# Optimization experiments

Measured on AMD Instinct MI355X. Metric: run time of the kernel, lower is better.

Reference implementation:

```python
import jax, jax.numpy as jnp
import numpy as np
from jax import lax

T, B, H_IN, H_HID = 2048, 64, 256, 256


def _orth(key, shape):
    a = jax.random.normal(key, shape, jnp.float32)
    if shape[0] >= shape[1]:
        q, _ = jnp.linalg.qr(a)
    else:
        q, _ = jnp.linalg.qr(a.T)
        q = q.T
    return q[: shape[0], : shape[1]].astype(jnp.float32)


def setup_inputs() -> dict:
    key = jax.random.key(0)
    ks = jax.random.split(key, 6)
    x = jax.random.normal(ks[0], (T, B, H_IN), jnp.float32)
    rnn_hxs = jax.random.normal(ks[1], (1, B, H_HID), jnp.float32)
    batch_mask = jax.random.randint(ks[2], (T, B), 0, 2).astype(bool)
    # force column 0 fully valid so pad_packed max length == T (static shape)
    batch_mask = batch_mask.at[:, 0].set(True)
    w_ih = _orth(ks[3], (3 * H_HID, H_IN))   # [3H, H_in] gates r,z,n
    w_hh = _orth(ks[4], (3 * H_HID, H_HID))
    b_ih = jnp.zeros((3 * H_HID,), jnp.float32)  # constant_(0) init
    b_hh = jnp.zeros((3 * H_HID,), jnp.float32)
    return {"x": x, "rnn_hxs": rnn_hxs, "batch_mask": batch_mask,
            "w_ih": w_ih, "w_hh": w_hh, "b_ih": b_ih, "b_hh": b_hh}


def _gru_ragged(x, h0, batch_mask, w_ih, w_hh, b_ih, b_hh):
    Tn, Bn, _ = x.shape
    Hh = h0.shape[-1]
    mask = batch_mask
    lens = mask.sum(0)                      # [B] per-column valid lengths
    # --- gather/pack: move valid steps of each column to the front ---
    rank = jnp.cumsum(mask, axis=0) - mask  # compact position per (t,b)
    rank_m = jnp.where(mask, rank, Tn)      # invalid rows -> dump row Tn
    cols = jnp.broadcast_to(jnp.arange(Bn), (Tn, Bn))
    compact = jnp.zeros((Tn + 1, Bn, x.shape[-1]), x.dtype)
    compact = compact.at[rank_m, cols].set(x)[:Tn]
    # --- GRU over compact sequences; h frozen past each column's length ---
    gi = jnp.einsum('tbi,gi->tbg', compact, w_ih) + b_ih  # [T,B,3H]
    valid = jnp.arange(Tn)[:, None] < lens[None, :]       # [T,B]

    def step(h, inp):
        gi_t, v = inp
        gh = jnp.einsum('bh,gh->bg', h, w_hh) + b_hh
        r = jax.nn.sigmoid(gi_t[:, :Hh] + gh[:, :Hh])
        z = jax.nn.sigmoid(gi_t[:, Hh:2 * Hh] + gh[:, Hh:2 * Hh])
        n = jnp.tanh(gi_t[:, 2 * Hh:] + r * gh[:, 2 * Hh:])
        h_new = (1.0 - z) * n + z * h
        h_out = jnp.where(v[:, None], h_new, h)
        out = jnp.where(v[:, None], h_new, 0.0)  # pad_packed zero padding
        return h_out, out

    hT, scores = lax.scan(step, h0, (gi, valid))  # scores [T,B,Hh]
    # --- masked_scatter: true positions of dest (row-major t,b order)
    # consume consecutive H-rows of the flattened padded scores ---
    mflat = mask.reshape(-1)
    flat_rank = jnp.cumsum(mflat) - mflat            # exclusive cumsum
    src = scores.reshape(Tn * Bn, Hh)
    gathered = src[flat_rank]                        # [T*B, Hh]
    out = jnp.where(mflat[:, None], gathered, 0.0).reshape(Tn, Bn, Hh)
    return out, hT


def reference(x, rnn_hxs, batch_mask, w_ih, w_hh, b_ih, b_hh):
    scores, hT = _gru_ragged(x, rnn_hxs[0], batch_mask, w_ih, w_hh, b_ih, b_hh)
    return scores, hT[None]
```

## Files before the change

### kernel.cpp

```cpp
#include <hip/hip_runtime.h>
#include <cstdint>
#include <cstddef>

#define T_LEN 2048
#define B_N   64
#define H_INP 256
#define H_HID 256
#define G3    768
#define M_ROWS (T_LEN * B_N)
#define SCH   16

typedef _Float16 f16;
typedef _Float16 f16x2 __attribute__((ext_vector_type(2)));
typedef _Float16 f16x8 __attribute__((ext_vector_type(8)));
typedef float    f32x4 __attribute__((ext_vector_type(4)));

static __device__ __forceinline__ float fdot2f(uint32_t a, uint32_t b, float c) {
#if __has_builtin(__builtin_amdgcn_fdot2)
  return __builtin_amdgcn_fdot2(__builtin_bit_cast(f16x2, a),
                                __builtin_bit_cast(f16x2, b), c, false);
#else
  f16x2 av = __builtin_bit_cast(f16x2, a);
  f16x2 bv = __builtin_bit_cast(f16x2, b);
  return c + (float)av.x * (float)bv.x + (float)av.y * (float)bv.y;
#endif
}

__global__ void k_zero(float4* __restrict__ p, int n4) {
  int i = blockIdx.x * blockDim.x + threadIdx.x;
  int stride = gridDim.x * blockDim.x;
  float4 z; z.x = z.y = z.z = z.w = 0.f;
  for (; i < n4; i += stride) p[i] = z;
}

__global__ void k_cvt(const float2* __restrict__ s, f16x2* __restrict__ d, int n2) {
  int i = blockIdx.x * blockDim.x + threadIdx.x;
  int stride = gridDim.x * blockDim.x;
  for (; i < n2; i += stride) {
    float2 v = s[i];
    f16x2 p; p.x = (f16)v.x; p.y = (f16)v.y;
    d[i] = p;
  }
}

__global__ __launch_bounds__(64) void k_prep_col(const int* __restrict__ mask,
                                                 unsigned short* __restrict__ tidx,
                                                 int* __restrict__ lens) {
  const int b = blockIdx.x;
  const int lane = threadIdx.x;
  unsigned short* tp = tidx + b * T_LEN;
  int base = 0;
  for (int c = 0; c < T_LEN / 64; ++c) {
    int t = c * 64 + lane;
    bool m = mask[t * B_N + b] != 0;
    unsigned long long bal = __ballot(m);
    int pc = __popcll(bal & ((1ull << lane) - 1ull));
    if (m) tp[base + pc] = (unsigned short)t;
    base += __popcll(bal);
  }
  if (lane == 0) lens[b] = base;
}

__global__ __launch_bounds__(256) void k_rowcnt(const int* __restrict__ mask,
                                                int* __restrict__ rowcnt) {
  int g = blockIdx.x * 256 + threadIdx.x;
  int t = g >> 6, lane = g & 63;
  bool m = mask[t * B_N + lane] != 0;
  unsigned long long bal = __ballot(m);
  if (lane == 0) rowcnt[t] = __popcll(bal);
}

__global__ __launch_bounds__(512) void k_rowpref(const int* __restrict__ rowcnt,
                                                 int* __restrict__ rowpref,
                                                 int* __restrict__ ntru) {
  const int tid = threadIdx.x;
  const int lane = tid & 63, w = tid >> 6;
  int4 v = ((const int4*)rowcnt)[tid];
  int s = v.x + v.y + v.z + v.w;
  int incl = s;
  for (int d = 1; d < 64; d <<= 1) {
    int t = __shfl_up(incl, d, 64);
    if (lane >= d) incl += t;
  }
  __shared__ int wt[8], wo[8];
  if (lane == 63) wt[w] = incl;
  __syncthreads();
  if (tid == 0) {
    int run = 0;
    for (int i = 0; i < 8; ++i) { wo[i] = run; run += wt[i]; }
    ntru[0] = run;
  }
  __syncthreads();
  int base = wo[w] + incl - s;
  int4 o; o.x = base; o.y = base + v.x; o.z = o.y + v.y; o.w = o.z + v.z;
  ((int4*)rowpref)[tid] = o;
}

__global__ __launch_bounds__(256) void k_inv(const int* __restrict__ mask,
                                             const int* __restrict__ rowpref,
                                             int* __restrict__ inv) {
  int g = blockIdx.x * 256 + threadIdx.x;
  int t = g >> 6, lane = g & 63;
  bool m = mask[t * B_N + lane] != 0;
  unsigned long long bal = __ballot(m);
  int r = rowpref[t] + __popcll(bal & ((1ull << lane) - 1ull));
  if (m) inv[r] = t * B_N + lane;
}

__global__ __launch_bounds__(256) void k_gemm(const f16* __restrict__ X,
                                              const f16* __restrict__ W,
                                              const float* __restrict__ bias,
                                              f16* __restrict__ GI) {
  const int lane = threadIdx.x & 63;
  const int wave = threadIdx.x >> 6;
  const int m0 = blockIdx.x * 64 + wave * 16;
  const int n0 = blockIdx.y * 64;
  const int idx16 = lane & 15;
  const int kofs  = (lane >> 4) * 8;

  const f16* ap  = X + (size_t)(m0 + idx16) * H_INP + kofs;
  const f16* bp0 = W + (size_t)(n0 + idx16) * H_INP + kofs;

  f32x4 acc[4] = { {0,0,0,0}, {0,0,0,0}, {0,0,0,0}, {0,0,0,0} };
#pragma unroll
  for (int kt = 0; kt < 8; ++kt) {
    f16x8 a = *(const f16x8*)(ap + kt * 32);
#pragma unroll
    for (int nt = 0; nt < 4; ++nt) {
      f16x8 bb = *(const f16x8*)(bp0 + (size_t)nt * 16 * H_INP + kt * 32);
      acc[nt] = __builtin_amdgcn_mfma_f32_16x16x32_f16(a, bb, acc[nt], 0, 0, 0);
    }
  }
  const int mbase = m0 + (lane >> 4) * 4;
#pragma unroll
  for (int nt = 0; nt < 4; ++nt) {
    const int col = n0 + nt * 16 + idx16;
    const float bv = bias[col];
#pragma unroll
    for (int r = 0; r < 4; ++r)
      GI[(size_t)(mbase + r) * G3 + col] = (f16)(acc[nt][r] + bv);
  }
}

__global__ __launch_bounds__(768, 3) void k_scan(const f16* __restrict__ Whh,
                                                 const f16* __restrict__ GI,
                                                 const float* __restrict__ h0,
                                                 const float* __restrict__ bhh,
                                                 const unsigned short* __restrict__ tidx,
                                                 const int* __restrict__ lens,
                                                 const int* __restrict__ inv,
                                                 const int* __restrict__ ntru,
                                                 float* __restrict__ out) {
  const int b = blockIdx.x;
  const int tid = threadIdx.x;
  const int lane = tid & 63;
  const int wav = tid >> 6;

  __shared__ f16   GIbuf[SCH * G3];
  __shared__ float outb[SCH * H_HID];
  __shared__ float ghs[2 * H_HID];
  __shared__ f16   hpk[H_HID];
  __shared__ int   ivb[2][SCH];

  uint32_t w[128];
  {
    const uint4* wp = (const uint4*)(Whh + (size_t)tid * H_HID);
#pragma unroll
    for (int i = 0; i < 32; ++i) {
      uint4 v = wp[i];
      w[4*i+0] = v.x; w[4*i+1] = v.y; w[4*i+2] = v.z; w[4*i+3] = v.w;
    }
  }
  const float bias = bhh[tid];
  float h_reg = 0.f;
  if (tid < H_HID) h_reg = h0[b * H_HID + tid];
  if (tid < H_HID / 2) {
    float2 hv = ((const float2*)(h0 + b * H_HID))[tid];
    f16x2 p; p.x = (f16)hv.x; p.y = (f16)hv.y;
    ((f16x2*)hpk)[tid] = p;
  }
  const int L  = lens[b];
  const int Nt = ntru[0];
  const unsigned short* tptr = tidx + b * T_LEN;
  __syncthreads();

  for (int k = 0; k < L; ++k) {
    if ((k & (SCH - 1)) == 0) {
      const int par = (k >> 4) & 1;
      if (k > 0) {
        for (int r = wav; r < SCH; r += 12) {
          int iv = ivb[par ^ 1][r];
          if (iv >= 0)
            *(float4*)(out + (size_t)iv * H_HID + (lane << 2)) =
                *(const float4*)(outb + r * H_HID + (lane << 2));
        }
      }
      {
        int nrows = L - k; if (nrows > SCH) nrows = SCH;
        int r = tid / 48, c = tid % 48;
        if (r < nrows) {
          int t = tptr[k + r];
          const uint4* src = (const uint4*)(GI + ((size_t)t * B_N + b) * G3) + (c << 1);
          uint4 v0 = src[0], v1 = src[1];
          uint4* dst = (uint4*)(GIbuf + r * G3) + (c << 1);
          dst[0] = v0; dst[1] = v1;
        }
        if (tid < SCH) {
          int kk = k + tid;
          int pr = kk * B_N + b;
          ivb[par][tid] = (kk < L && pr < Nt) ? inv[pr] : -1;
        }
      }
      __syncthreads();
    }
    float acc0 = bias, acc1 = 0.f;
    {
      const uint4* hb = (const uint4*)hpk;
#pragma unroll
      for (int i = 0; i < 16; ++i) {
        uint4 hv = hb[i];
        acc0 = fdot2f(w[4*i+0], hv.x, acc0);
        acc0 = fdot2f(w[4*i+1], hv.y, acc0);
        acc0 = fdot2f(w[4*i+2], hv.z, acc0);
        acc0 = fdot2f(w[4*i+3], hv.w, acc0);
      }
#pragma unroll
      for (int i = 16; i < 32; ++i) {
        uint4 hv = hb[i];
        acc1 = fdot2f(w[4*i+0], hv.x, acc1);
        acc1 = fdot2f(w[4*i+1], hv.y, acc1);
        acc1 = fdot2f(w[4*i+2], hv.z, acc1);
        acc1 = fdot2f(w[4*i+3], hv.w, acc1);
      }
    }
    const float gh = acc0 + acc1;
    if (tid >= H_HID) ghs[tid - H_HID] = gh;
    __syncthreads();
    if (tid < H_HID) {
      const int slot = k & (SCH - 1);
      const float gi0 = (float)GIbuf[slot * G3 + tid];
      const float gi1 = (float)GIbuf[slot * G3 + H_HID + tid];
      const float gi2 = (float)GIbuf[slot * G3 + 2 * H_HID + tid];
      const float ghz = ghs[tid];
      const float ghn = ghs[H_HID + tid];
      const float rg = __builtin_amdgcn_rcpf(1.f + __expf(-(gi0 + gh)));
      const float zg = __builtin_amdgcn_rcpf(1.f + __expf(-(gi1 + ghz)));
      const float xx = gi2 + rg * ghn;
      const float ng = 1.f - 2.f * __builtin_amdgcn_rcpf(1.f + __expf(2.f * xx));
      const float hn = (1.f - zg) * ng + zg * h_reg;
      h_reg = hn;
      hpk[tid] = (f16)hn;
      outb[slot * H_HID + tid] = hn;
    }
    __syncthreads();
  }
  if (L > 0) {
    const int kb = (L - 1) & ~(SCH - 1);
    const int rows = L - kb;
    const int par = (kb >> 4) & 1;
    for (int r = wav; r < rows; r += 12) {
      int iv = ivb[par][r];
      if (iv >= 0)
        *(float4*)(out + (size_t)iv * H_HID + (lane << 2)) =
            *(const float4*)(outb + r * H_HID + (lane << 2));
    }
  }
  if (tid < H_HID)
    out[(size_t)M_ROWS * H_HID + (size_t)b * H_HID + tid] = h_reg;
}

extern "C" void kernel_launch(void* const* d_in, const int* in_sizes, int n_in,
                              void* d_out, int out_size, void* d_ws, size_t ws_size,
                              hipStream_t stream) {
  const float* x    = (const float*)d_in[0];
  const float* h0   = (const float*)d_in[1];
  const int*   mask = (const int*)d_in[2];
  const float* wih  = (const float*)d_in[3];
  const float* whh  = (const float*)d_in[4];
  const float* bih  = (const float*)d_in[5];
  const float* bhh  = (const float*)d_in[6];
  float* out = (float*)d_out;

  char* ws = (char*)d_ws;
  f16* X16   = (f16*)(ws + 0);
  f16* Wih16 = (f16*)(ws + 67108864);
  f16* Whh16 = (f16*)(ws + 67502080);
  f16* GI    = (f16*)(ws + 67895296);
  unsigned short* tidx = (unsigned short*)(ws + 269221888);
  int* rowcnt  = (int*)(ws + 269484032);
  int* rowpref = (int*)(ws + 269492224);
  int* inv   = (int*)(ws + 269746176);
  int* lens  = (int*)(ws + 270270464);
  int* ntru  = (int*)(ws + 270270720);

  hipLaunchKernelGGL(k_zero, dim3(4096), dim3(256), 0, stream,
                     (float4*)d_out, out_size / 4);
  hipLaunchKernelGGL(k_cvt, dim3(4096), dim3(256), 0, stream,
                     (const float2*)x, (f16x2*)X16, M_ROWS * H_INP / 2);
  hipLaunchKernelGGL(k_cvt, dim3(96), dim3(256), 0, stream,
                     (const float2*)wih, (f16x2*)Wih16, G3 * H_INP / 2);
  hipLaunchKernelGGL(k_cvt, dim3(96), dim3(256), 0, stream,
                     (const float2*)whh, (f16x2*)Whh16, G3 * H_INP / 2);
  hipLaunchKernelGGL(k_prep_col, dim3(B_N), dim3(64), 0, stream,
                     mask, tidx, lens);
  hipLaunchKernelGGL(k_rowcnt, dim3(512), dim3(256), 0, stream, mask, rowcnt);
  hipLaunchKernelGGL(k_rowpref, dim3(1), dim3(512), 0, stream,
                     rowcnt, rowpref, ntru);
  hipLaunchKernelGGL(k_inv, dim3(512), dim3(256), 0, stream,
                     mask, rowpref, inv);
  hipLaunchKernelGGL(k_gemm, dim3(M_ROWS / 64, G3 / 64), dim3(256), 0, stream,
                     X16, Wih16, bih, GI);
  hipLaunchKernelGGL(k_scan, dim3(B_N), dim3(768), 0, stream,
                     Whh16, GI, h0, bhh, tidx, lens, inv, ntru, out);
}
```

Before: 3.310 ms.

## Restructure GRU scan with split-K matvec, GI register prefetch and staged index tables

The recurrent matvec is redistributed so each thread holds a 32-column slice of 8 weight rows and reduces across 8 lanes with shuffles. This reads the h vector from a padded LDS layout to cut bank conflicts and replaces per-thread full-row dot products. GI rows for the next chunk are prefetched into registers and double-buffered in LDS, so global loads overlap the serial steps. The scatter indices are transposed per column by a new kernel and, together with the time indices, preloaded into LDS. The chunk size is halved, the shuffle reduction adds cross-lane latency on the serial critical path, and invT reuses the X16 workspace after the GEMM.

```diff
diff --git a/kernel.cpp b/kernel.cpp
--- a/kernel.cpp
+++ b/kernel.cpp
@@ -8,7 +8,7 @@
 #define H_HID 256
 #define G3    768
 #define M_ROWS (T_LEN * B_N)
-#define SCH   16
+#define SCH   8
 
 typedef _Float16 f16;
 typedef _Float16 f16x2 __attribute__((ext_vector_type(2)));
@@ -107,6 +107,14 @@
   if (m) inv[r] = t * B_N + lane;
 }
 
+__global__ __launch_bounds__(256) void k_invT(const int* __restrict__ inv,
+                                              const int* __restrict__ ntru,
+                                              int* __restrict__ invT) {
+  int j = blockIdx.x * 256 + threadIdx.x;
+  int v = (j < ntru[0]) ? inv[j] : -1;
+  invT[(j & 63) * T_LEN + (j >> 6)] = v;
+}
+
 __global__ __launch_bounds__(256) void k_gemm(const f16* __restrict__ X,
                                               const f16* __restrict__ W,
                                               const float* __restrict__ bias,
@@ -148,121 +156,138 @@
                                                  const float* __restrict__ bhh,
                                                  const unsigned short* __restrict__ tidx,
                                                  const int* __restrict__ lens,
-                                                 const int* __restrict__ inv,
-                                                 const int* __restrict__ ntru,
+                                                 const int* __restrict__ invT,
                                                  float* __restrict__ out) {
   const int b = blockIdx.x;
   const int tid = threadIdx.x;
-  const int lane = tid & 63;
-  const int wav = tid >> 6;
-
-  __shared__ f16   GIbuf[SCH * G3];
-  __shared__ float outb[SCH * H_HID];
-  __shared__ float ghs[2 * H_HID];
-  __shared__ f16   hpk[H_HID];
-  __shared__ int   ivb[2][SCH];
-
-  uint32_t w[128];
-  {
-    const uint4* wp = (const uint4*)(Whh + (size_t)tid * H_HID);
-#pragma unroll
-    for (int i = 0; i < 32; ++i) {
-      uint4 v = wp[i];
-      w[4*i+0] = v.x; w[4*i+1] = v.y; w[4*i+2] = v.z; w[4*i+3] = v.w;
-    }
+  const int o = tid & 7;
+  const int rbase = (tid >> 3) << 3;
+
+  __shared__ f16      GIbuf[2][SCH * G3];
+  __shared__ float    outb[SCH * H_HID];
+  __shared__ float    ghs[2 * H_HID];
+  __shared__ uint32_t hpad[160];
+  __shared__ unsigned short tcol[T_LEN];
+  __shared__ int      invcol[T_LEN];
+
+  const int L = lens[b];
+
+  uint4 wq[8][4];
+#pragma unroll
+  for (int i = 0; i < 8; ++i) {
+    const uint4* wp = (const uint4*)(Whh + (size_t)(rbase + i) * H_HID + 32 * o);
+#pragma unroll
+    for (int q = 0; q < 4; ++q) wq[i][q] = wp[q];
   }
   const float bias = bhh[tid];
+
+  for (int i = tid; i < T_LEN; i += 768) {
+    tcol[i] = tidx[b * T_LEN + i];
+    invcol[i] = invT[b * T_LEN + i];
+  }
   float h_reg = 0.f;
-  if (tid < H_HID) h_reg = h0[b * H_HID + tid];
-  if (tid < H_HID / 2) {
-    float2 hv = ((const float2*)(h0 + b * H_HID))[tid];
-    f16x2 p; p.x = (f16)hv.x; p.y = (f16)hv.y;
-    ((f16x2*)hpk)[tid] = p;
-  }
-  const int L  = lens[b];
-  const int Nt = ntru[0];
-  const unsigned short* tptr = tidx + b * T_LEN;
+  if (tid < H_HID) {
+    h_reg = h0[b * H_HID + tid];
+    ((f16*)hpad)[40 * (tid >> 5) + (tid & 31)] = (f16)h_reg;
+  }
+
+  const int r_s = tid / 96;
+  const int o_s = (tid % 96) * 16;
+  const char* GIc = (const char*)GI;
+  uint4 pref = {0, 0, 0, 0};
+
   __syncthreads();
 
-  for (int k = 0; k < L; ++k) {
-    if ((k & (SCH - 1)) == 0) {
-      const int par = (k >> 4) & 1;
-      if (k > 0) {
-        for (int r = wav; r < SCH; r += 12) {
-          int iv = ivb[par ^ 1][r];
-          if (iv >= 0)
-            *(float4*)(out + (size_t)iv * H_HID + (lane << 2)) =
-                *(const float4*)(outb + r * H_HID + (lane << 2));
-        }
+  if (r_s < L) {
+    int t = tcol[r_s];
+    pref = *(const uint4*)(GIc + ((size_t)t * B_N + b) * (G3 * 2) + o_s);
+  }
+
+  const int nchunks = (L + SCH - 1) >> 3;
+  for (int n = 0; n < nchunks; ++n) {
+    const int par = n & 1;
+    if (n * SCH + r_s < L)
+      *(uint4*)((char*)GIbuf[par] + tid * 16) = pref;
+    {
+      int kk = (n + 1) * SCH + r_s;
+      if (kk < L) {
+        int t = tcol[kk];
+        pref = *(const uint4*)(GIc + ((size_t)t * B_N + b) * (G3 * 2) + o_s);
       }
-      {
-        int nrows = L - k; if (nrows > SCH) nrows = SCH;
-        int r = tid / 48, c = tid % 48;
-        if (r < nrows) {
-          int t = tptr[k + r];
-          const uint4* src = (const uint4*)(GI + ((size_t)t * B_N + b) * G3) + (c << 1);
-          uint4 v0 = src[0], v1 = src[1];
-          uint4* dst = (uint4*)(GIbuf + r * G3) + (c << 1);
-          dst[0] = v0; dst[1] = v1;
-        }
-        if (tid < SCH) {
-          int kk = k + tid;
-          int pr = kk * B_N + b;
-          ivb[par][tid] = (kk < L && pr < Nt) ? inv[pr] : -1;
-        }
+    }
+    if (n > 0 && tid < 512) {
+      int r = tid >> 6, c4 = (tid & 63) << 2;
+      int kk = (n - 1) * SCH + r;
+      if (kk < L) {
+        int iv = invcol[kk];
+        if (iv >= 0)
+          *(float4*)(out + (size_t)iv * H_HID + c4) = *(const float4*)(outb + r * H_HID + c4);
+      }
+    }
+
+    const int smax = (L - n * SCH < SCH) ? (L - n * SCH) : SCH;
+    for (int s = 0; s < smax; ++s) {
+      float a0 = 0.f, a1 = 0.f, a2 = 0.f, a3 = 0.f;
+      float a4 = 0.f, a5 = 0.f, a6 = 0.f, a7 = 0.f;
+#pragma unroll
+      for (int q = 0; q < 4; ++q) {
+        uint4 hv = *(const uint4*)(hpad + 20 * o + 4 * q);
+        a0 = fdot2f(wq[0][q].x, hv.x, a0); a0 = fdot2f(wq[0][q].y, hv.y, a0);
+        a0 = fdot2f(wq[0][q].z, hv.z, a0); a0 = fdot2f(wq[0][q].w, hv.w, a0);
+        a1 = fdot2f(wq[1][q].x, hv.x, a1); a1 = fdot2f(wq[1][q].y, hv.y, a1);
+        a1 = fdot2f(wq[1][q].z, hv.z, a1); a1 = fdot2f(wq[1][q].w, hv.w, a1);
+        a2 = fdot2f(wq[2][q].x, hv.x, a2); a2 = fdot2f(wq[2][q].y, hv.y, a2);
+        a2 = fdot2f(wq[2][q].z, hv.z, a2); a2 = fdot2f(wq[2][q].w, hv.w, a2);
+        a3 = fdot2f(wq[3][q].x, hv.x, a3); a3 = fdot2f(wq[3][q].y, hv.y, a3);
+        a3 = fdot2f(wq[3][q].z, hv.z, a3); a3 = fdot2f(wq[3][q].w, hv.w, a3);
+        a4 = fdot2f(wq[4][q].x, hv.x, a4); a4 = fdot2f(wq[4][q].y, hv.y, a4);
+        a4 = fdot2f(wq[4][q].z, hv.z, a4); a4 = fdot2f(wq[4][q].w, hv.w, a4);
+        a5 = fdot2f(wq[5][q].x, hv.x, a5); a5 = fdot2f(wq[5][q].y, hv.y, a5);
+        a5 = fdot2f(wq[5][q].z, hv.z, a5); a5 = fdot2f(wq[5][q].w, hv.w, a5);
+        a6 = fdot2f(wq[6][q].x, hv.x, a6); a6 = fdot2f(wq[6][q].y, hv.y, a6);
+        a6 = fdot2f(wq[6][q].z, hv.z, a6); a6 = fdot2f(wq[6][q].w, hv.w, a6);
+        a7 = fdot2f(wq[7][q].x, hv.x, a7); a7 = fdot2f(wq[7][q].y, hv.y, a7);
+        a7 = fdot2f(wq[7][q].z, hv.z, a7); a7 = fdot2f(wq[7][q].w, hv.w, a7);
+      }
+      const bool h4 = (tid & 4), h2 = (tid & 2), h1 = (tid & 1);
+      float se, ns, b0, b1, b2, b3, c0, c1;
+      se = h4 ? a4 : a0; ns = h4 ? a0 : a4; b0 = se + __shfl_xor(ns, 4);
+      se = h4 ? a5 : a1; ns = h4 ? a1 : a5; b1 = se + __shfl_xor(ns, 4);
+      se = h4 ? a6 : a2; ns = h4 ? a2 : a6; b2 = se + __shfl_xor(ns, 4);
+      se = h4 ? a7 : a3; ns = h4 ? a3 : a7; b3 = se + __shfl_xor(ns, 4);
+      se = h2 ? b2 : b0; ns = h2 ? b0 : b2; c0 = se + __shfl_xor(ns, 2);
+      se = h2 ? b3 : b1; ns = h2 ? b1 : b3; c1 = se + __shfl_xor(ns, 2);
+      se = h1 ? c1 : c0; ns = h1 ? c0 : c1;
+      const float gh = se + __shfl_xor(ns, 1) + bias;
+      if (tid >= H_HID) ghs[tid - H_HID] = gh;
+      __syncthreads();
+      if (tid < H_HID) {
+        const f16* gib = GIbuf[par] + s * G3;
+        const float gi0 = (float)gib[tid];
+        const float gi1 = (float)gib[H_HID + tid];
+        const float gi2 = (float)gib[2 * H_HID + tid];
+        const float ghz = ghs[tid];
+        const float ghn = ghs[H_HID + tid];
+        const float rg = __builtin_amdgcn_rcpf(1.f + __expf(-(gi0 + gh)));
+        const float zg = __builtin_amdgcn_rcpf(1.f + __expf(-(gi1 + ghz)));
+        const float xx = gi2 + rg * ghn;
+        const float ng = 1.f - 2.f * __builtin_amdgcn_rcpf(1.f + __expf(2.f * xx));
+        const float hn = (1.f - zg) * ng + zg * h_reg;
+        h_reg = hn;
+        ((f16*)hpad)[40 * (tid >> 5) + (tid & 31)] = (f16)hn;
+        outb[s * H_HID + tid] = hn;
       }
       __syncthreads();
     }
-    float acc0 = bias, acc1 = 0.f;
-    {
-      const uint4* hb = (const uint4*)hpk;
-#pragma unroll
-      for (int i = 0; i < 16; ++i) {
-        uint4 hv = hb[i];
-        acc0 = fdot2f(w[4*i+0], hv.x, acc0);
-        acc0 = fdot2f(w[4*i+1], hv.y, acc0);
-        acc0 = fdot2f(w[4*i+2], hv.z, acc0);
-        acc0 = fdot2f(w[4*i+3], hv.w, acc0);
-      }
-#pragma unroll
-      for (int i = 16; i < 32; ++i) {
-        uint4 hv = hb[i];
-        acc1 = fdot2f(w[4*i+0], hv.x, acc1);
-        acc1 = fdot2f(w[4*i+1], hv.y, acc1);
-        acc1 = fdot2f(w[4*i+2], hv.z, acc1);
-        acc1 = fdot2f(w[4*i+3], hv.w, acc1);
-      }
-    }
-    const float gh = acc0 + acc1;
-    if (tid >= H_HID) ghs[tid - H_HID] = gh;
-    __syncthreads();
-    if (tid < H_HID) {
-      const int slot = k & (SCH - 1);
-      const float gi0 = (float)GIbuf[slot * G3 + tid];
-      const float gi1 = (float)GIbuf[slot * G3 + H_HID + tid];
-      const float gi2 = (float)GIbuf[slot * G3 + 2 * H_HID + tid];
-      const float ghz = ghs[tid];
-      const float ghn = ghs[H_HID + tid];
-      const float rg = __builtin_amdgcn_rcpf(1.f + __expf(-(gi0 + gh)));
-      const float zg = __builtin_amdgcn_rcpf(1.f + __expf(-(gi1 + ghz)));
-      const float xx = gi2 + rg * ghn;
-      const float ng = 1.f - 2.f * __builtin_amdgcn_rcpf(1.f + __expf(2.f * xx));
-      const float hn = (1.f - zg) * ng + zg * h_reg;
-      h_reg = hn;
-      hpk[tid] = (f16)hn;
-      outb[slot * H_HID + tid] = hn;
-    }
-    __syncthreads();
-  }
-  if (L > 0) {
-    const int kb = (L - 1) & ~(SCH - 1);
-    const int rows = L - kb;
-    const int par = (kb >> 4) & 1;
-    for (int r = wav; r < rows; r += 12) {
-      int iv = ivb[par][r];
+  }
+  if (L > 0 && tid < 512) {
+    const int nc = nchunks - 1;
+    int r = tid >> 6, c4 = (tid & 63) << 2;
+    int kk = nc * SCH + r;
+    if (kk < L) {
+      int iv = invcol[kk];
       if (iv >= 0)
-        *(float4*)(out + (size_t)iv * H_HID + (lane << 2)) =
-            *(const float4*)(outb + r * H_HID + (lane << 2));
+        *(float4*)(out + (size_t)iv * H_HID + c4) = *(const float4*)(outb + r * H_HID + c4);
     }
   }
   if (tid < H_HID)
@@ -283,6 +308,7 @@
 
   char* ws = (char*)d_ws;
   f16* X16   = (f16*)(ws + 0);
+  int* invT  = (int*)(ws + 0);
   f16* Wih16 = (f16*)(ws + 67108864);
   f16* Whh16 = (f16*)(ws + 67502080);
   f16* GI    = (f16*)(ws + 67895296);
@@ -310,6 +336,8 @@
                      mask, rowpref, inv);
   hipLaunchKernelGGL(k_gemm, dim3(M_ROWS / 64, G3 / 64), dim3(256), 0, stream,
                      X16, Wih16, bih, GI);
+  hipLaunchKernelGGL(k_invT, dim3(512), dim3(256), 0, stream,
+                     inv, ntru, invT);
   hipLaunchKernelGGL(k_scan, dim3(B_N), dim3(768), 0, stream,
-                     Whh16, GI, h0, bhh, tidx, lens, inv, ntru, out);
-}
+                     Whh16, GI, h0, bhh, tidx, lens, invT, out);
+}
```

New measurement: 3.413 ms. +3.1%, slower.
